# Kernel tuning notes

Measured on AMD Instinct MI355X. Metric: run time of the kernel, lower is better.

The kernel has to match this reference:

```python
import jax, jax.numpy as jnp
import numpy as np

N = 50000       # nodes
E = 500000      # directed edges
Q_EDGES = 100000
F_IN = 128
HID = 64
K = 2           # Chebyshev order -> K+1 weight slices
LABEL = 2
Q_PHASE = 0.25
TWO_PI = 2.0 * np.pi


def setup_inputs() -> dict:
    key = jax.random.key(0)
    ks = jax.random.split(key, 9)
    real = jax.random.normal(ks[0], (N, F_IN), jnp.float32)
    imag = jax.random.normal(ks[1], (N, F_IN), jnp.float32)
    src = jax.random.randint(ks[2], (E,), 0, N)
    off = jax.random.randint(ks[3], (E,), 1, N)
    dst = (src + off) % N  # no self loops (torch code removes them)
    edge_index = jnp.stack([src, dst]).astype(jnp.int64)
    query_edges = jax.random.randint(ks[4], (Q_EDGES, 2), 0, N).astype(jnp.int64)
    edge_weight = jax.random.uniform(ks[5], (E,), jnp.float32, 0.5, 1.5)
    W1 = jax.random.normal(ks[6], (K + 1, F_IN, HID), jnp.float32) / np.sqrt(F_IN)
    b1 = jnp.zeros((HID,), jnp.float32)
    W2 = jax.random.normal(ks[7], (K + 1, HID, HID), jnp.float32) / np.sqrt(HID)
    b2 = jnp.zeros((HID,), jnp.float32)
    Wlin = jax.random.normal(ks[8], (LABEL, 4 * HID), jnp.float32) / np.sqrt(4 * HID)
    blin = jnp.zeros((LABEL,), jnp.float32)
    return dict(real=real, imag=imag, edge_index=edge_index, query_edges=query_edges,
                edge_weight=edge_weight, W1=W1, b1=b1, W2=W2, b2=b2, Wlin=Wlin, blin=blin)


def magnetic_norm(edge_index, edge_weight, num_nodes, q):
    """Edge weights of scaled magnetic Laplacian L_hat = L - I (sym norm, lambda_max=2).

    Returns symmetrized edge list (2E edges) with real/imag coefficients
    -D^{-1/2} A_s D^{-1/2} * exp(i * theta), theta = 2*pi*q*(A - A^T).
    """
    u, v = edge_index[0], edge_index[1]
    s = jnp.concatenate([u, v])                  # source (j)
    d = jnp.concatenate([v, u])                  # target (i)
    w_sym = jnp.concatenate([edge_weight, edge_weight]) * 0.5  # A_s = (A + A^T)/2
    theta = TWO_PI * q * jnp.concatenate([edge_weight, -edge_weight])
    deg = jax.ops.segment_sum(w_sym, s, num_segments=num_nodes)
    dinv = jnp.where(deg > 0, jax.lax.rsqrt(jnp.where(deg > 0, deg, 1.0)), 0.0)
    norm = dinv[s] * w_sym * dinv[d]
    return s, d, -norm * jnp.cos(theta), -norm * jnp.sin(theta)


def magnet_conv(xr, xi, s, d, nr, ni, W, b, num_nodes):
    def prop(x, c):  # out[i] = sum_{e: d_e = i} c_e * x[s_e]
        return jax.ops.segment_sum(c[:, None] * x[s], d, num_segments=num_nodes)

    xs = (xr, xi, xr, xi)            # streams: real_real, imag_imag, imag_real, real_imag
    cs = (nr, ni, ni, nr)            # norm used by each stream
    T0 = xs
    out = [x @ W[0] for x in T0]
    T1 = tuple(prop(x, c) for x, c in zip(xs, cs))
    out = [o + t @ W[1] for o, t in zip(out, T1)]
    for k in range(2, W.shape[0]):
        T2 = tuple(2.0 * prop(t1, c) - t0 for t0, t1, c in zip(T0, T1, cs))
        out = [o + t @ W[k] for o, t in zip(out, T2)]
        T0, T1 = T1, T2
    out_r = out[0] - out[1] + b
    out_i = out[2] + out[3] + b
    return out_r, out_i


def complex_relu(xr, xi):
    mask = (xr >= 0).astype(xr.dtype)
    return xr * mask, xi * mask


def reference(real, imag, edge_index, query_edges, edge_weight, W1, b1, W2, b2, Wlin, blin):
    num_nodes = real.shape[0]
    s, d, nr, ni = magnetic_norm(edge_index, edge_weight, num_nodes, Q_PHASE)
    xr, xi = magnet_conv(real, imag, s, d, nr, ni, W1, b1, num_nodes)
    xr, xi = complex_relu(xr, xi)
    xr, xi = magnet_conv(xr, xi, s, d, nr, ni, W2, b2, num_nodes)
    xr, xi = complex_relu(xr, xi)
    q0, q1 = query_edges[:, 0], query_edges[:, 1]
    x = jnp.concatenate([xr[q0], xr[q1], xi[q0], xi[q1]], axis=-1)  # [Q, 4*hidden]
    # dropout is identity in eval mode
    logits = x @ Wlin.T + blin
    return jax.nn.log_softmax(logits, axis=1)
```

## Files before the change

### kernel.cpp

```cpp
#include <hip/hip_runtime.h>


__device__ __forceinline__ float4 ld4(const float* __restrict__ p) {
  return *reinterpret_cast<const float4*>(p);
}
__device__ __forceinline__ float2 ld2(const float* __restrict__ p) {
  return *reinterpret_cast<const float2*>(p);
}

__global__ void k_deg_count(const int* __restrict__ u, const int* __restrict__ v,
                            const float* __restrict__ w,
                            unsigned long long* __restrict__ dc, int E) {
  int e = blockIdx.x * 256 + threadIdx.x;
  if (e >= E) return;
  float hw = 0.5f * w[e];
  unsigned fx = __float2uint_rn(hw * 16777216.f);
  unsigned long long pk = (1ULL << 32) | (unsigned long long)fx;
  atomicAdd(&dc[u[e]], pk);
  atomicAdd(&dc[v[e]], pk);
}

__global__ __launch_bounds__(256) void k_scan1(
    const unsigned long long* __restrict__ dc, int* __restrict__ rp,
    int* __restrict__ bsum, int N) {
  __shared__ int sh[256];
  int t = threadIdx.x;
  int base = blockIdx.x * 1024 + t * 4;
  int c0 = (base + 0 < N) ? (int)(dc[base + 0] >> 32) : 0;
  int c1 = (base + 1 < N) ? (int)(dc[base + 1] >> 32) : 0;
  int c2 = (base + 2 < N) ? (int)(dc[base + 2] >> 32) : 0;
  int c3 = (base + 3 < N) ? (int)(dc[base + 3] >> 32) : 0;
  int s = c0 + c1 + c2 + c3;
  sh[t] = s;
  __syncthreads();
  for (int o = 1; o < 256; o <<= 1) {
    int y = (t >= o) ? sh[t - o] : 0;
    __syncthreads();
    if (t >= o) sh[t] += y;
    __syncthreads();
  }
  int excl = sh[t] - s;
  if (base + 0 < N) rp[base + 0] = excl;
  if (base + 1 < N) rp[base + 1] = excl + c0;
  if (base + 2 < N) rp[base + 2] = excl + c0 + c1;
  if (base + 3 < N) rp[base + 3] = excl + c0 + c1 + c2;
  if (t == 255) bsum[blockIdx.x] = sh[255];
}

__global__ void k_scan2(int* __restrict__ bsum, int NB) {
  if (threadIdx.x == 0 && blockIdx.x == 0) {
    int run = 0;
    for (int i = 0; i < NB; ++i) { int x = bsum[i]; bsum[i] = run; run += x; }
  }
}

__global__ void k_scan3(int* __restrict__ rp, int* __restrict__ nxt,
                        const int* __restrict__ bsum, int N, int twoE) {
  int i = blockIdx.x * 256 + threadIdx.x;
  if (i < N) {
    int val = rp[i] + bsum[i >> 10];
    rp[i] = val;
    nxt[i] = val;
  } else if (i == N) {
    rp[N] = twoE;
  }
}

__global__ void k_scatter(const int* __restrict__ u, const int* __restrict__ v,
                          const float* __restrict__ w,
                          const unsigned long long* __restrict__ dc,
                          int* __restrict__ nxt, int* __restrict__ src,
                          float2* __restrict__ cf, int E) {
  int e = blockIdx.x * 256 + threadIdx.x;
  if (e >= E) return;
  int a = u[e], b = v[e];
  float we = w[e];
  float da = (float)(unsigned)dc[a] * (1.f / 16777216.f);
  float db = (float)(unsigned)dc[b] * (1.f / 16777216.f);
  float ia = da > 0.f ? rsqrtf(da) : 0.f;
  float ib = db > 0.f ? rsqrtf(db) : 0.f;
  float norm = ia * (0.5f * we) * ib;
  float th = 1.57079632679489662f * we;
  float sn, cs;
  sincosf(th, &sn, &cs);
  float cr = -norm * cs, ci = -norm * sn;
  int p1 = atomicAdd(&nxt[b], 1);
  src[p1] = a;
  cf[p1] = make_float2(cr, ci);
  int p2 = atomicAdd(&nxt[a], 1);
  src[p2] = b;
  cf[p2] = make_float2(cr, -ci);
}

template <int K>
__global__ __launch_bounds__(256) void k_gemmF(
    const float* __restrict__ Ar, const float* __restrict__ Ai,
    const float* __restrict__ W,
    const float* __restrict__ bias,
    float* __restrict__ P1, float* __restrict__ P2,
    float* __restrict__ Hr, float* __restrict__ Hi, int M) {
  __shared__ float Asr[64][20];
  __shared__ float Asi[64][20];
  __shared__ float Ws1[16][64];
  __shared__ float Ws2[16][64];
  __shared__ float Wsm[16][64];
  const int t = threadIdx.x;
  const int r0 = blockIdx.x * 64;
  const int tc = t & 15, tr = t >> 4;
  const float* W0 = W;
  const float* W1 = W + (size_t)K * 64;
  const float* W2 = W + (size_t)2 * K * 64;
  float a1r[4][4] = {}, a1i[4][4] = {}, a2r[4][4] = {}, a2i[4][4] = {};
  float amr[4][4] = {}, ami[4][4] = {};
  for (int k0 = 0; k0 < K; k0 += 16) {
    {
      int row = t >> 2, c4 = t & 3;
      int gr = r0 + row;
      float4 fr = make_float4(0.f, 0.f, 0.f, 0.f), fi = fr;
      if (gr < M) {
        fr = ld4(&Ar[(size_t)gr * K + k0 + c4 * 4]);
        fi = ld4(&Ai[(size_t)gr * K + k0 + c4 * 4]);
      }
      *reinterpret_cast<float4*>(&Asr[row][c4 * 4]) = fr;
      *reinterpret_cast<float4*>(&Asi[row][c4 * 4]) = fi;
    }
    {
      int row = t >> 4, c4 = t & 15;
      size_t woff = (size_t)(k0 + row) * 64 + c4 * 4;
      float4 w1 = ld4(&W1[woff]);
      float4 w2 = ld4(&W2[woff]);
      float4 w0 = ld4(&W0[woff]);
      *reinterpret_cast<float4*>(&Ws1[row][c4 * 4]) = w1;
      *reinterpret_cast<float4*>(&Ws2[row][c4 * 4]) = w2;
      *reinterpret_cast<float4*>(&Wsm[row][c4 * 4]) =
          make_float4(w0.x - w2.x, w0.y - w2.y, w0.z - w2.z, w0.w - w2.w);
    }
    __syncthreads();
#pragma unroll 4
    for (int k = 0; k < 16; ++k) {
      float4 b1 = *reinterpret_cast<const float4*>(&Ws1[k][tc * 4]);
      float4 b2 = *reinterpret_cast<const float4*>(&Ws2[k][tc * 4]);
      float4 bm = *reinterpret_cast<const float4*>(&Wsm[k][tc * 4]);
#pragma unroll
      for (int i = 0; i < 4; ++i) {
        float ar = Asr[tr * 4 + i][k], ai = Asi[tr * 4 + i][k];
        a1r[i][0] += ar * b1.x; a1r[i][1] += ar * b1.y; a1r[i][2] += ar * b1.z; a1r[i][3] += ar * b1.w;
        a1i[i][0] += ai * b1.x; a1i[i][1] += ai * b1.y; a1i[i][2] += ai * b1.z; a1i[i][3] += ai * b1.w;
        a2r[i][0] += ar * b2.x; a2r[i][1] += ar * b2.y; a2r[i][2] += ar * b2.z; a2r[i][3] += ar * b2.w;
        a2i[i][0] += ai * b2.x; a2i[i][1] += ai * b2.y; a2i[i][2] += ai * b2.z; a2i[i][3] += ai * b2.w;
        amr[i][0] += ar * bm.x; amr[i][1] += ar * bm.y; amr[i][2] += ar * bm.z; amr[i][3] += ar * bm.w;
        ami[i][0] += ai * bm.x; ami[i][1] += ai * bm.y; ami[i][2] += ai * bm.z; ami[i][3] += ai * bm.w;
      }
    }
    __syncthreads();
  }
  float b0 = bias[tc * 4 + 0], bb1 = bias[tc * 4 + 1];
  float b2v = bias[tc * 4 + 2], b3 = bias[tc * 4 + 3];
#pragma unroll
  for (int i = 0; i < 4; ++i) {
    int gr = r0 + tr * 4 + i;
    if (gr >= M) continue;
    size_t pb = (size_t)gr * 128 + tc * 8;
    *reinterpret_cast<float4*>(&P1[pb]) =
        make_float4(a1r[i][0], a1i[i][0], a1r[i][1], a1i[i][1]);
    *reinterpret_cast<float4*>(&P1[pb + 4]) =
        make_float4(a1r[i][2], a1i[i][2], a1r[i][3], a1i[i][3]);
    *reinterpret_cast<float4*>(&P2[pb]) =
        make_float4(a2r[i][0], a2i[i][0], a2r[i][1], a2i[i][1]);
    *reinterpret_cast<float4*>(&P2[pb + 4]) =
        make_float4(a2r[i][2], a2i[i][2], a2r[i][3], a2i[i][3]);
    size_t hb = (size_t)gr * 64 + tc * 4;
    *reinterpret_cast<float4*>(&Hr[hb]) =
        make_float4(amr[i][0] - ami[i][0] + b0, amr[i][1] - ami[i][1] + bb1,
                    amr[i][2] - ami[i][2] + b2v, amr[i][3] - ami[i][3] + b3);
    *reinterpret_cast<float4*>(&Hi[hb]) =
        make_float4(amr[i][0] + ami[i][0] + b0, amr[i][1] + ami[i][1] + bb1,
                    amr[i][2] + ami[i][2] + b2v, amr[i][3] + ami[i][3] + b3);
  }
}

__global__ __launch_bounds__(256) void k_gU(
    const int* __restrict__ src, const float2* __restrict__ cf,
    const int* __restrict__ rp, const float* __restrict__ P2,
    float* __restrict__ U1, float* __restrict__ U2, int N) {
  int d = blockIdx.x * 4 + (threadIdx.x >> 6);
  if (d >= N) return;
  int lane = threadIdx.x & 63;
  int g = lane >> 5, lg = lane & 31;
  float4 a01 = {0, 0, 0, 0};
  float4 a23 = {0, 0, 0, 0};
  int k1 = rp[d + 1];
#pragma unroll 2
  for (int k = rp[d] + g; k < k1; k += 2) {
    int s = src[k];
    float2 c = cf[k];
    float4 v = ld4(P2 + (size_t)s * 128 + lg * 4);
    a01.x += c.x * v.x; a01.y += c.y * v.y;
    a01.z += c.x * v.z; a01.w += c.y * v.w;
    a23.x += c.y * v.x; a23.y += c.x * v.y;
    a23.z += c.y * v.z; a23.w += c.x * v.w;
  }
  a01.x += __shfl_xor(a01.x, 32); a01.y += __shfl_xor(a01.y, 32);
  a01.z += __shfl_xor(a01.z, 32); a01.w += __shfl_xor(a01.w, 32);
  a23.x += __shfl_xor(a23.x, 32); a23.y += __shfl_xor(a23.y, 32);
  a23.z += __shfl_xor(a23.z, 32); a23.w += __shfl_xor(a23.w, 32);
  size_t ub = (size_t)d * 128 + lg * 4;
  if (g == 0)
    *reinterpret_cast<float4*>(&U1[ub]) = a01;
  else
    *reinterpret_cast<float4*>(&U2[ub]) = a23;
}

__global__ void k_comb(const float* __restrict__ P1, float* __restrict__ U1,
                       float* __restrict__ U2, int n4) {
  int i = blockIdx.x * 256 + threadIdx.x;
  if (i >= n4) return;
  float4 p = ld4(P1 + (size_t)i * 4);
  float4 a = ld4(U1 + (size_t)i * 4);
  float4 b = ld4(U2 + (size_t)i * 4);
  *reinterpret_cast<float4*>(&U1[(size_t)i * 4]) =
      make_float4(p.x + 2.f * a.x, p.y + 2.f * a.y, p.z + 2.f * a.z, p.w + 2.f * a.w);
  *reinterpret_cast<float4*>(&U2[(size_t)i * 4]) =
      make_float4(p.x + 2.f * b.x, p.y + 2.f * b.y, p.z + 2.f * b.z, p.w + 2.f * b.w);
}

__global__ __launch_bounds__(256) void k_gC1(
    const int* __restrict__ src, const float2* __restrict__ cf,
    const int* __restrict__ rp, const float* __restrict__ Z1,
    float* __restrict__ Hr, int N) {
  int d = blockIdx.x * 4 + (threadIdx.x >> 6);
  if (d >= N) return;
  int lane = threadIdx.x & 63;
  int g = lane >> 5, lg = lane & 31;
  float2 acc = {0, 0};
  int k1 = rp[d + 1];
#pragma unroll 2
  for (int k = rp[d] + g; k < k1; k += 2) {
    int s = src[k];
    float2 c = cf[k];
    float4 v = ld4(Z1 + (size_t)s * 128 + lg * 4);
    acc.x += c.x * v.x - c.y * v.y;
    acc.y += c.x * v.z - c.y * v.w;
  }
  acc.x += __shfl_xor(acc.x, 32);
  acc.y += __shfl_xor(acc.y, 32);
  if (g == 0) {
    size_t hb = (size_t)d * 64 + lg * 2;
    float2 h = ld2(&Hr[hb]);
    *reinterpret_cast<float2*>(&Hr[hb]) = make_float2(h.x + acc.x, h.y + acc.y);
  }
}

__global__ __launch_bounds__(256) void k_gC2(
    const int* __restrict__ src, const float2* __restrict__ cf,
    const int* __restrict__ rp, const float* __restrict__ Z2,
    float* __restrict__ Hr, float* __restrict__ Hi, int N) {
  int d = blockIdx.x * 4 + (threadIdx.x >> 6);
  if (d >= N) return;
  int lane = threadIdx.x & 63;
  int g = lane >> 5, lg = lane & 31;
  float2 acc = {0, 0};
  int k1 = rp[d + 1];
#pragma unroll 2
  for (int k = rp[d] + g; k < k1; k += 2) {
    int s = src[k];
    float2 c = cf[k];
    float4 v = ld4(Z2 + (size_t)s * 128 + lg * 4);
    acc.x += c.y * v.x + c.x * v.y;
    acc.y += c.y * v.z + c.x * v.w;
  }
  acc.x += __shfl_xor(acc.x, 32);
  acc.y += __shfl_xor(acc.y, 32);
  if (g == 0) {
    size_t hb = (size_t)d * 64 + lg * 2;
    float2 hr = ld2(&Hr[hb]);
    float2 hi = ld2(&Hi[hb]);
    hi.x += acc.x;
    hi.y += acc.y;
    if (hr.x < 0.f) { hr.x = 0.f; hi.x = 0.f; }
    if (hr.y < 0.f) { hr.y = 0.f; hi.y = 0.f; }
    *reinterpret_cast<float2*>(&Hr[hb]) = hr;
    *reinterpret_cast<float2*>(&Hi[hb]) = hi;
  }
}

__global__ __launch_bounds__(256) void k_query(
    const int* __restrict__ qe, const float* __restrict__ xr,
    const float* __restrict__ xi, const float* __restrict__ Wlin,
    const float* __restrict__ blin, float* __restrict__ out, int Q) {
  int q = blockIdx.x * 4 + (threadIdx.x >> 6);
  if (q >= Q) return;
  int lane = threadIdx.x & 63;
  int q0 = qe[2 * q], q1 = qe[2 * q + 1];
  float x0 = xr[(size_t)q0 * 64 + lane];
  float x1 = xr[(size_t)q1 * 64 + lane];
  float x2 = xi[(size_t)q0 * 64 + lane];
  float x3 = xi[(size_t)q1 * 64 + lane];
  float l0 = x0 * Wlin[lane] + x1 * Wlin[64 + lane] + x2 * Wlin[128 + lane] + x3 * Wlin[192 + lane];
  float l1 = x0 * Wlin[256 + lane] + x1 * Wlin[320 + lane] + x2 * Wlin[384 + lane] + x3 * Wlin[448 + lane];
#pragma unroll
  for (int o = 32; o > 0; o >>= 1) {
    l0 += __shfl_xor(l0, o);
    l1 += __shfl_xor(l1, o);
  }
  if (lane == 0) {
    l0 += blin[0];
    l1 += blin[1];
    float m = fmaxf(l0, l1);
    float lse = m + logf(expf(l0 - m) + expf(l1 - m));
    out[2 * q + 0] = l0 - lse;
    out[2 * q + 1] = l1 - lse;
  }
}

extern "C" void kernel_launch(void* const* d_in, const int* in_sizes, int n_in,
                              void* d_out, int out_size, void* d_ws, size_t ws_size,
                              hipStream_t stream) {
  const float* real = (const float*)d_in[0];
  const float* imag = (const float*)d_in[1];
  const int* ei     = (const int*)d_in[2];
  const int* qe     = (const int*)d_in[3];
  const float* ew   = (const float*)d_in[4];
  const float* W1   = (const float*)d_in[5];
  const float* b1   = (const float*)d_in[6];
  const float* W2   = (const float*)d_in[7];
  const float* b2   = (const float*)d_in[8];
  const float* Wlin = (const float*)d_in[9];
  const float* blin = (const float*)d_in[10];

  const int N = in_sizes[0] / 128;
  const int E = in_sizes[4];
  const int Q = in_sizes[3] / 2;
  const int* u = ei;
  const int* v = ei + E;

  float* ws = (float*)d_ws;
  size_t off = 0;
  auto alloc = [&](size_t n) { float* p = ws + off; off += n; return p; };
  const size_t N64 = (size_t)N * 64;
  const size_t N128 = (size_t)N * 128;

  float2* cf = (float2*)alloc((size_t)2 * E * 2);
  unsigned long long* dc = (unsigned long long*)alloc((size_t)2 * N);
  int* src  = (int*)alloc((size_t)2 * E);
  float* P1  = alloc(N128);
  float* P2  = alloc(N128);
  float* U1  = alloc(N128);
  float* U2  = alloc(N128);
  float* HAr = alloc(N64);
  float* HAi = alloc(N64);
  float* HBr = alloc(N64);
  float* HBi = alloc(N64);
  int* rp   = (int*)alloc(N + 1);
  int* nxt  = (int*)alloc(N);
  int* bsum = (int*)alloc(64);
  (void)ws_size; (void)n_in; (void)out_size;

  const int eb = (E + 255) / 256;
  const int mb = (N + 63) / 64;
  const int NB = (N + 1023) / 1024;
  const int gb = (N + 3) / 4;
  const int n4 = (int)(N128 / 4);
  const int cb = (n4 + 255) / 256;

  hipMemsetAsync(dc, 0, (size_t)N * 8, stream);
  k_deg_count<<<eb, 256, 0, stream>>>(u, v, ew, dc, E);
  k_scan1<<<NB, 256, 0, stream>>>(dc, rp, bsum, N);
  k_scan2<<<1, 64, 0, stream>>>(bsum, NB);
  k_scan3<<<(N + 256) / 256, 256, 0, stream>>>(rp, nxt, bsum, N, 2 * E);
  k_scatter<<<eb, 256, 0, stream>>>(u, v, ew, dc, nxt, src, cf, E);

  k_gemmF<128><<<mb, 256, 0, stream>>>(real, imag, W1, b1, P1, P2, HAr, HAi, N);
  k_gU<<<gb, 256, 0, stream>>>(src, cf, rp, P2, U1, U2, N);
  k_comb<<<cb, 256, 0, stream>>>(P1, U1, U2, n4);
  k_gC1<<<gb, 256, 0, stream>>>(src, cf, rp, U1, HAr, N);
  k_gC2<<<gb, 256, 0, stream>>>(src, cf, rp, U2, HAr, HAi, N);

  k_gemmF<64><<<mb, 256, 0, stream>>>(HAr, HAi, W2, b2, P1, P2, HBr, HBi, N);
  k_gU<<<gb, 256, 0, stream>>>(src, cf, rp, P2, U1, U2, N);
  k_comb<<<cb, 256, 0, stream>>>(P1, U1, U2, n4);
  k_gC1<<<gb, 256, 0, stream>>>(src, cf, rp, U1, HBr, N);
  k_gC2<<<gb, 256, 0, stream>>>(src, cf, rp, U2, HBr, HBi, N);

  k_query<<<(Q + 3) / 4, 256, 0, stream>>>(qe, HBr, HBi, Wlin, blin, (float*)d_out, Q);
}
```

Before: 737.9 us.

## Fuse combine into gather, merge two gather passes, retile GEMM to 32 rows

The elementwise combine kernel is folded into the first gather kernel, which now reads P1 and writes P1+2*acc directly into an interleaved Z buffer (256 floats per node). The two second-stage gather kernels are merged into one that reads both halves of each Z row and updates Hr and Hi together. This removes a full pass over the N×128 arrays and one redundant walk over the edge list per layer. The GEMM tile is changed to 32 rows with K-step 32, giving more blocks and fewer accumulators per thread, at the cost of less reuse of each weight load.

```diff
diff --git a/kernel.cpp b/kernel.cpp
--- a/kernel.cpp
+++ b/kernel.cpp
@@ -99,22 +99,22 @@
     const float* __restrict__ bias,
     float* __restrict__ P1, float* __restrict__ P2,
     float* __restrict__ Hr, float* __restrict__ Hi, int M) {
-  __shared__ float Asr[64][20];
-  __shared__ float Asi[64][20];
-  __shared__ float Ws1[16][64];
-  __shared__ float Ws2[16][64];
-  __shared__ float Wsm[16][64];
+  __shared__ float Asr[32][36];
+  __shared__ float Asi[32][36];
+  __shared__ float Ws1[32][64];
+  __shared__ float Ws2[32][64];
+  __shared__ float Wsm[32][64];
   const int t = threadIdx.x;
-  const int r0 = blockIdx.x * 64;
+  const int r0 = blockIdx.x * 32;
   const int tc = t & 15, tr = t >> 4;
   const float* W0 = W;
   const float* W1 = W + (size_t)K * 64;
   const float* W2 = W + (size_t)2 * K * 64;
-  float a1r[4][4] = {}, a1i[4][4] = {}, a2r[4][4] = {}, a2i[4][4] = {};
-  float amr[4][4] = {}, ami[4][4] = {};
-  for (int k0 = 0; k0 < K; k0 += 16) {
+  float a1r[2][4] = {}, a1i[2][4] = {}, a2r[2][4] = {}, a2i[2][4] = {};
+  float amr[2][4] = {}, ami[2][4] = {};
+  for (int k0 = 0; k0 < K; k0 += 32) {
     {
-      int row = t >> 2, c4 = t & 3;
+      int row = t >> 3, c4 = t & 7;
       int gr = r0 + row;
       float4 fr = make_float4(0.f, 0.f, 0.f, 0.f), fi = fr;
       if (gr < M) {
@@ -124,8 +124,8 @@
       *reinterpret_cast<float4*>(&Asr[row][c4 * 4]) = fr;
       *reinterpret_cast<float4*>(&Asi[row][c4 * 4]) = fi;
     }
-    {
-      int row = t >> 4, c4 = t & 15;
+    for (int li = t; li < 512; li += 256) {
+      int row = li >> 4, c4 = li & 15;
       size_t woff = (size_t)(k0 + row) * 64 + c4 * 4;
       float4 w1 = ld4(&W1[woff]);
       float4 w2 = ld4(&W2[woff]);
@@ -137,13 +137,13 @@
     }
     __syncthreads();
 #pragma unroll 4
-    for (int k = 0; k < 16; ++k) {
+    for (int k = 0; k < 32; ++k) {
       float4 b1 = *reinterpret_cast<const float4*>(&Ws1[k][tc * 4]);
       float4 b2 = *reinterpret_cast<const float4*>(&Ws2[k][tc * 4]);
       float4 bm = *reinterpret_cast<const float4*>(&Wsm[k][tc * 4]);
 #pragma unroll
-      for (int i = 0; i < 4; ++i) {
-        float ar = Asr[tr * 4 + i][k], ai = Asi[tr * 4 + i][k];
+      for (int i = 0; i < 2; ++i) {
+        float ar = Asr[tr * 2 + i][k], ai = Asi[tr * 2 + i][k];
         a1r[i][0] += ar * b1.x; a1r[i][1] += ar * b1.y; a1r[i][2] += ar * b1.z; a1r[i][3] += ar * b1.w;
         a1i[i][0] += ai * b1.x; a1i[i][1] += ai * b1.y; a1i[i][2] += ai * b1.z; a1i[i][3] += ai * b1.w;
         a2r[i][0] += ar * b2.x; a2r[i][1] += ar * b2.y; a2r[i][2] += ar * b2.z; a2r[i][3] += ar * b2.w;
@@ -157,8 +157,8 @@
   float b0 = bias[tc * 4 + 0], bb1 = bias[tc * 4 + 1];
   float b2v = bias[tc * 4 + 2], b3 = bias[tc * 4 + 3];
 #pragma unroll
-  for (int i = 0; i < 4; ++i) {
-    int gr = r0 + tr * 4 + i;
+  for (int i = 0; i < 2; ++i) {
+    int gr = r0 + tr * 2 + i;
     if (gr >= M) continue;
     size_t pb = (size_t)gr * 128 + tc * 8;
     *reinterpret_cast<float4*>(&P1[pb]) =
@@ -182,7 +182,7 @@
 __global__ __launch_bounds__(256) void k_gU(
     const int* __restrict__ src, const float2* __restrict__ cf,
     const int* __restrict__ rp, const float* __restrict__ P2,
-    float* __restrict__ U1, float* __restrict__ U2, int N) {
+    const float* __restrict__ P1, float* __restrict__ Z, int N) {
   int d = blockIdx.x * 4 + (threadIdx.x >> 6);
   if (d >= N) return;
   int lane = threadIdx.x & 63;
@@ -204,79 +204,50 @@
   a01.z += __shfl_xor(a01.z, 32); a01.w += __shfl_xor(a01.w, 32);
   a23.x += __shfl_xor(a23.x, 32); a23.y += __shfl_xor(a23.y, 32);
   a23.z += __shfl_xor(a23.z, 32); a23.w += __shfl_xor(a23.w, 32);
-  size_t ub = (size_t)d * 128 + lg * 4;
+  float4 p = ld4(P1 + (size_t)d * 128 + lg * 4);
+  size_t zb = (size_t)d * 256 + lg * 4;
   if (g == 0)
-    *reinterpret_cast<float4*>(&U1[ub]) = a01;
+    *reinterpret_cast<float4*>(&Z[zb]) =
+        make_float4(p.x + 2.f * a01.x, p.y + 2.f * a01.y,
+                    p.z + 2.f * a01.z, p.w + 2.f * a01.w);
   else
-    *reinterpret_cast<float4*>(&U2[ub]) = a23;
-}
-
-__global__ void k_comb(const float* __restrict__ P1, float* __restrict__ U1,
-                       float* __restrict__ U2, int n4) {
-  int i = blockIdx.x * 256 + threadIdx.x;
-  if (i >= n4) return;
-  float4 p = ld4(P1 + (size_t)i * 4);
-  float4 a = ld4(U1 + (size_t)i * 4);
-  float4 b = ld4(U2 + (size_t)i * 4);
-  *reinterpret_cast<float4*>(&U1[(size_t)i * 4]) =
-      make_float4(p.x + 2.f * a.x, p.y + 2.f * a.y, p.z + 2.f * a.z, p.w + 2.f * a.w);
-  *reinterpret_cast<float4*>(&U2[(size_t)i * 4]) =
-      make_float4(p.x + 2.f * b.x, p.y + 2.f * b.y, p.z + 2.f * b.z, p.w + 2.f * b.w);
-}
-
-__global__ __launch_bounds__(256) void k_gC1(
+    *reinterpret_cast<float4*>(&Z[zb + 128]) =
+        make_float4(p.x + 2.f * a23.x, p.y + 2.f * a23.y,
+                    p.z + 2.f * a23.z, p.w + 2.f * a23.w);
+}
+
+__global__ __launch_bounds__(256) void k_gC(
     const int* __restrict__ src, const float2* __restrict__ cf,
-    const int* __restrict__ rp, const float* __restrict__ Z1,
-    float* __restrict__ Hr, int N) {
+    const int* __restrict__ rp, const float* __restrict__ Z,
+    float* __restrict__ Hr, float* __restrict__ Hi, int N) {
   int d = blockIdx.x * 4 + (threadIdx.x >> 6);
   if (d >= N) return;
   int lane = threadIdx.x & 63;
   int g = lane >> 5, lg = lane & 31;
-  float2 acc = {0, 0};
+  float2 ahr = {0, 0}, ahi = {0, 0};
   int k1 = rp[d + 1];
 #pragma unroll 2
   for (int k = rp[d] + g; k < k1; k += 2) {
     int s = src[k];
     float2 c = cf[k];
-    float4 v = ld4(Z1 + (size_t)s * 128 + lg * 4);
-    acc.x += c.x * v.x - c.y * v.y;
-    acc.y += c.x * v.z - c.y * v.w;
-  }
-  acc.x += __shfl_xor(acc.x, 32);
-  acc.y += __shfl_xor(acc.y, 32);
-  if (g == 0) {
-    size_t hb = (size_t)d * 64 + lg * 2;
-    float2 h = ld2(&Hr[hb]);
-    *reinterpret_cast<float2*>(&Hr[hb]) = make_float2(h.x + acc.x, h.y + acc.y);
-  }
-}
-
-__global__ __launch_bounds__(256) void k_gC2(
-    const int* __restrict__ src, const float2* __restrict__ cf,
-    const int* __restrict__ rp, const float* __restrict__ Z2,
-    float* __restrict__ Hr, float* __restrict__ Hi, int N) {
-  int d = blockIdx.x * 4 + (threadIdx.x >> 6);
-  if (d >= N) return;
-  int lane = threadIdx.x & 63;
-  int g = lane >> 5, lg = lane & 31;
-  float2 acc = {0, 0};
-  int k1 = rp[d + 1];
-#pragma unroll 2
-  for (int k = rp[d] + g; k < k1; k += 2) {
-    int s = src[k];
-    float2 c = cf[k];
-    float4 v = ld4(Z2 + (size_t)s * 128 + lg * 4);
-    acc.x += c.y * v.x + c.x * v.y;
-    acc.y += c.y * v.z + c.x * v.w;
-  }
-  acc.x += __shfl_xor(acc.x, 32);
-  acc.y += __shfl_xor(acc.y, 32);
+    const float* row = Z + (size_t)s * 256 + lg * 4;
+    float4 z1 = ld4(row);
+    float4 z2 = ld4(row + 128);
+    ahr.x += c.x * z1.x - c.y * z1.y;
+    ahr.y += c.x * z1.z - c.y * z1.w;
+    ahi.x += c.y * z2.x + c.x * z2.y;
+    ahi.y += c.y * z2.z + c.x * z2.w;
+  }
+  ahr.x += __shfl_xor(ahr.x, 32);
+  ahr.y += __shfl_xor(ahr.y, 32);
+  ahi.x += __shfl_xor(ahi.x, 32);
+  ahi.y += __shfl_xor(ahi.y, 32);
   if (g == 0) {
     size_t hb = (size_t)d * 64 + lg * 2;
     float2 hr = ld2(&Hr[hb]);
     float2 hi = ld2(&Hi[hb]);
-    hi.x += acc.x;
-    hi.y += acc.y;
+    hr.x += ahr.x; hr.y += ahr.y;
+    hi.x += ahi.x; hi.y += ahi.y;
     if (hr.x < 0.f) { hr.x = 0.f; hi.x = 0.f; }
     if (hr.y < 0.f) { hr.y = 0.f; hi.y = 0.f; }
     *reinterpret_cast<float2*>(&Hr[hb]) = hr;
@@ -339,14 +310,14 @@
   auto alloc = [&](size_t n) { float* p = ws + off; off += n; return p; };
   const size_t N64 = (size_t)N * 64;
   const size_t N128 = (size_t)N * 128;
+  const size_t N256 = (size_t)N * 256;
 
   float2* cf = (float2*)alloc((size_t)2 * E * 2);
   unsigned long long* dc = (unsigned long long*)alloc((size_t)2 * N);
   int* src  = (int*)alloc((size_t)2 * E);
   float* P1  = alloc(N128);
   float* P2  = alloc(N128);
-  float* U1  = alloc(N128);
-  float* U2  = alloc(N128);
+  float* Z   = alloc(N256);
   float* HAr = alloc(N64);
   float* HAi = alloc(N64);
   float* HBr = alloc(N64);
@@ -357,11 +328,9 @@
   (void)ws_size; (void)n_in; (void)out_size;
 
   const int eb = (E + 255) / 256;
-  const int mb = (N + 63) / 64;
+  const int mb = (N + 31) / 32;
   const int NB = (N + 1023) / 1024;
   const int gb = (N + 3) / 4;
-  const int n4 = (int)(N128 / 4);
-  const int cb = (n4 + 255) / 256;
 
   hipMemsetAsync(dc, 0, (size_t)N * 8, stream);
   k_deg_count<<<eb, 256, 0, stream>>>(u, v, ew, dc, E);
@@ -371,16 +340,12 @@
   k_scatter<<<eb, 256, 0, stream>>>(u, v, ew, dc, nxt, src, cf, E);
 
   k_gemmF<128><<<mb, 256, 0, stream>>>(real, imag, W1, b1, P1, P2, HAr, HAi, N);
-  k_gU<<<gb, 256, 0, stream>>>(src, cf, rp, P2, U1, U2, N);
-  k_comb<<<cb, 256, 0, stream>>>(P1, U1, U2, n4);
-  k_gC1<<<gb, 256, 0, stream>>>(src, cf, rp, U1, HAr, N);
-  k_gC2<<<gb, 256, 0, stream>>>(src, cf, rp, U2, HAr, HAi, N);
+  k_gU<<<gb, 256, 0, stream>>>(src, cf, rp, P2, P1, Z, N);
+  k_gC<<<gb, 256, 0, stream>>>(src, cf, rp, Z, HAr, HAi, N);
 
   k_gemmF<64><<<mb, 256, 0, stream>>>(HAr, HAi, W2, b2, P1, P2, HBr, HBi, N);
-  k_gU<<<gb, 256, 0, stream>>>(src, cf, rp, P2, U1, U2, N);
-  k_comb<<<cb, 256, 0, stream>>>(P1, U1, U2, n4);
-  k_gC1<<<gb, 256, 0, stream>>>(src, cf, rp, U1, HBr, N);
-  k_gC2<<<gb, 256, 0, stream>>>(src, cf, rp, U2, HBr, HBi, N);
+  k_gU<<<gb, 256, 0, stream>>>(src, cf, rp, P2, P1, Z, N);
+  k_gC<<<gb, 256, 0, stream>>>(src, cf, rp, Z, HBr, HBi, N);
 
   k_query<<<(Q + 3) / 4, 256, 0, stream>>>(qe, HBr, HBi, Wlin, blin, (float*)d_out, Q);
 }
```

Result: faster. 685.7 us (-7.1%).
